# Kernel optimization log

Hardware: AMD Instinct MI355X
Metric: run time of the kernel (lower is better)

Reference implementation:

```python
import jax, jax.numpy as jnp
import numpy as np

TEMPERATURE = 0.5
NEG_FILL = -9e15


def setup_inputs() -> dict:
    key = jax.random.key(0)
    k1, k2 = jax.random.split(key)
    B, D = 8192, 128
    z_i = jax.random.normal(k1, (B, D), dtype=jnp.float32)
    z_j = jax.random.normal(k2, (B, D), dtype=jnp.float32)
    return {"z_i": z_i, "z_j": z_j}


def reference(z_i, z_j):
    B = z_i.shape[0]
    N = 2 * B
    z = jnp.concatenate([z_i, z_j], axis=0)              # [2B, D]
    sim = jnp.matmul(z, z.T) / TEMPERATURE               # [2B, 2B]
    # mask out self-similarity on the diagonal
    diag = jnp.eye(N, dtype=bool)
    sim = jnp.where(diag, NEG_FILL, sim)
    # positive pair of row k is row (k+B) mod 2B
    labels = jnp.concatenate([jnp.arange(B, N), jnp.arange(0, B)])
    # CrossEntropyLoss(reduction='sum'): sum_k logsumexp(sim[k]) - sim[k, labels[k]]
    lse = jax.nn.logsumexp(sim, axis=1)                  # [2B]
    pos = sim[jnp.arange(N), labels]                     # [2B]
    loss = jnp.sum(lse - pos)
    return loss / N
```

## Files before the change

### kernel.cpp

```cpp
#include <hip/hip_runtime.h>

#define TEMP    0.5f
#define LOG2E   1.4426950408889634f
#define C2      (LOG2E / TEMP)
#define MSHIFT  160.0f
#define LN2     0.6931471805599453f
#define NROWS   16384
#define BHALF   8192
#define DDIM    128
#define PREPB   2048

typedef __bf16 bf16x8 __attribute__((ext_vector_type(8)));
typedef float  f32x16 __attribute__((ext_vector_type(16)));
typedef float  f32x2  __attribute__((ext_vector_type(2)));

__device__ __forceinline__ float fexp2(float x) {
#if __has_builtin(__builtin_amdgcn_exp2f)
  return __builtin_amdgcn_exp2f(x);
#else
  return exp2f(x);
#endif
}

__device__ __forceinline__ unsigned short f2bf(float f) {
  unsigned int u = __float_as_uint(f);
  unsigned int r = (u + 0x7FFFu + ((u >> 16) & 1u)) >> 16;
  return (unsigned short)r;
}


__global__ void k_prep(const float* __restrict__ zi, const float* __restrict__ zj,
                       unsigned short* __restrict__ zbF,
                       float* __restrict__ S, float* __restrict__ Pp) {
  const int t   = blockIdx.x * 256 + threadIdx.x;
  const int row = t >> 5;
  const int k0  = (t & 31) * 4;
  const float* src = (row < BHALF) ? (zi + (size_t)row * DDIM)
                                   : (zj + (size_t)(row - BHALF) * DDIM);
  float4 v = *reinterpret_cast<const float4*>(src + k0);

  const int g = row >> 5, lo = row & 31, khi = k0 >> 3, j0 = k0 & 7;
  ushort4 o;
  o.x = f2bf(v.x); o.y = f2bf(v.y); o.z = f2bf(v.z); o.w = f2bf(v.w);
  *reinterpret_cast<ushort4*>(zbF + (size_t)g * 4096 + khi * 256 + lo * 8 + j0) = o;

  float dot = 0.f;
  if (row < BHALF) {
    float4 w = *reinterpret_cast<const float4*>(zj + (size_t)row * DDIM + k0);
    dot = fmaf(v.x, w.x, fmaf(v.y, w.y, fmaf(v.z, w.z, v.w * w.w)));
  }
#pragma unroll
  for (int m = 32; m >= 1; m >>= 1) dot += __shfl_xor(dot, m, 64);
  __shared__ float red[4];
  if ((threadIdx.x & 63) == 0) red[threadIdx.x >> 6] = dot;
  __syncthreads();
  if (threadIdx.x == 0) Pp[blockIdx.x] = red[0] + red[1] + red[2] + red[3];

  if (t < NROWS) S[t] = 0.f;
}

template <bool MASK>
__device__ __forceinline__ void expAcc(const f32x16& acc, f32x2& s, int d, int hi) {
#pragma unroll
  for (int k = 0; k < 8; ++k) {
    f32x2 u;
    u.x = acc[2 * k];
    u.y = acc[2 * k + 1];
    const f32x2 c2v = {C2, C2};
    const f32x2 msv = {-MSHIFT, -MSHIFT};
    u = __builtin_elementwise_fma(u, c2v, msv);
    f32x2 e;
    e.x = fexp2(u.x);
    e.y = fexp2(u.y);
    if (MASK) {
      const int r0 = 2 * k, r1 = 2 * k + 1;
      if (((r0 & 3) + 8 * (r0 >> 2) + 4 * hi) == d) e.x = 0.f;
      if (((r1 & 3) + 8 * (r1 >> 2) + 4 * hi) == d) e.y = 0.f;
    }
    s += e;
  }
}

__global__ __launch_bounds__(256, 2)
void k_main(const unsigned short* __restrict__ zbF, float* __restrict__ S) {
  const int wave = threadIdx.x >> 6;
  const int lane = threadIdx.x & 63;
  const int lo = lane & 31;
  const int hi = lane >> 5;
  const int rb = blockIdx.x & 31;
  const int cc = blockIdx.x >> 5;
  const int row0w = rb * 512 + wave * 128;

  bf16x8 b[4][8];
#pragma unroll
  for (int rt = 0; rt < 4; ++rt) {
    const unsigned short* bp = zbF + (size_t)((row0w >> 5) + rt) * 4096 + hi * 256 + lo * 8;
#pragma unroll
    for (int ks = 0; ks < 8; ++ks)
      b[rt][ks] = *reinterpret_cast<const bf16x8*>(bp + ks * 512);
  }

  const f32x16 kZ = {};
  f32x2 s[4];
#pragma unroll
  for (int rt = 0; rt < 4; ++rt) { s[rt].x = 0.f; s[rt].y = 0.f; }

  const int c0base = cc * 1024;
  const unsigned short* abase = zbF + (size_t)(c0base >> 5) * 4096 + hi * 256 + lo * 8;

  bf16x8 a[8];
#pragma unroll
  for (int ks = 0; ks < 8; ++ks)
    a[ks] = *reinterpret_cast<const bf16x8*>(abase + ks * 512);

  if (((blockIdx.x ^ wave) & 1) != 0) __builtin_amdgcn_s_sleep(4);

  for (int it = 0; it < 32; ++it) {
    const int c0 = c0base + it * 32;
    const int dr = c0 - row0w;
    const bool dg = (unsigned)dr < 128u;
    const int rtd = dg ? (dr >> 5) : -1;

    __builtin_amdgcn_s_setprio(1);
    f32x16 acc0 = __builtin_amdgcn_mfma_f32_32x32x16_bf16(a[0], b[0][0], kZ, 0, 0, 0);
    f32x16 acc1 = __builtin_amdgcn_mfma_f32_32x32x16_bf16(a[0], b[1][0], kZ, 0, 0, 0);
#pragma unroll
    for (int ks = 1; ks < 8; ++ks) {
      acc0 = __builtin_amdgcn_mfma_f32_32x32x16_bf16(a[ks], b[0][ks], acc0, 0, 0, 0);
      acc1 = __builtin_amdgcn_mfma_f32_32x32x16_bf16(a[ks], b[1][ks], acc1, 0, 0, 0);
    }
    __builtin_amdgcn_s_setprio(0);
    if (!dg) {
      expAcc<false>(acc0, s[0], -1, hi);
      expAcc<false>(acc1, s[1], -1, hi);
    } else {
      expAcc<true>(acc0, s[0], rtd == 0 ? lo : -1, hi);
      expAcc<true>(acc1, s[1], rtd == 1 ? lo : -1, hi);
    }

    __builtin_amdgcn_s_setprio(1);
    acc0 = __builtin_amdgcn_mfma_f32_32x32x16_bf16(a[0], b[2][0], kZ, 0, 0, 0);
    acc1 = __builtin_amdgcn_mfma_f32_32x32x16_bf16(a[0], b[3][0], kZ, 0, 0, 0);
#pragma unroll
    for (int ks = 1; ks < 8; ++ks) {
      acc0 = __builtin_amdgcn_mfma_f32_32x32x16_bf16(a[ks], b[2][ks], acc0, 0, 0, 0);
      acc1 = __builtin_amdgcn_mfma_f32_32x32x16_bf16(a[ks], b[3][ks], acc1, 0, 0, 0);
    }
    __builtin_amdgcn_s_setprio(0);

    if (it + 1 < 32) {
      const unsigned short* ap = abase + (size_t)(it + 1) * 4096;
#pragma unroll
      for (int ks = 0; ks < 8; ++ks)
        a[ks] = *reinterpret_cast<const bf16x8*>(ap + ks * 512);
    }

    if (!dg) {
      expAcc<false>(acc0, s[2], -1, hi);
      expAcc<false>(acc1, s[3], -1, hi);
    } else {
      expAcc<true>(acc0, s[2], rtd == 2 ? lo : -1, hi);
      expAcc<true>(acc1, s[3], rtd == 3 ? lo : -1, hi);
    }
  }

#pragma unroll
  for (int rt = 0; rt < 4; ++rt) {
    float v = s[rt].x + s[rt].y;
    v += __shfl_xor(v, 32, 64);
    if (hi == 0) atomicAdd(&S[row0w + rt * 32 + lo], v);
  }
}

__global__ void k_fin(const float* __restrict__ S, const float* __restrict__ Pp,
                      float* __restrict__ out) {
  const int t = threadIdx.x;
  float q = 0.f;
  for (int r = t; r < NROWS; r += 1024)
    q += LN2 * (MSHIFT + __log2f(S[r]));
  for (int r = t; r < PREPB; r += 1024)
    q -= 4.0f * Pp[r];
  __shared__ float red[1024];
  red[t] = q;
  __syncthreads();
  for (int s2 = 512; s2 > 0; s2 >>= 1) {
    if (t < s2) red[t] += red[t + s2];
    __syncthreads();
  }
  if (t == 0) out[0] = red[0] / (float)NROWS;
}

extern "C" void kernel_launch(void* const* d_in, const int* in_sizes, int n_in,
                              void* d_out, int out_size, void* d_ws, size_t ws_size,
                              hipStream_t stream) {
  const float* zi = (const float*)d_in[0];
  const float* zj = (const float*)d_in[1];
  unsigned short* zbF = (unsigned short*)d_ws;
  float* S  = (float*)((char*)d_ws + (size_t)NROWS * DDIM * 2);
  float* Pp = S + NROWS;
  float* out = (float*)d_out;

  hipLaunchKernelGGL(k_prep, dim3(PREPB), dim3(256), 0, stream, zi, zj, zbF, S, Pp);
  hipLaunchKernelGGL(k_main, dim3(512),  dim3(256), 0, stream, zbF, S);
  hipLaunchKernelGGL(k_fin,  dim3(1),    dim3(1024), 0, stream, S, Pp, out);
}
```

Baseline: 130.6 us.

## Fold scale into bf16 inputs, bias into MFMA init, and interleave MFMA with exp

The prep kernel now pre-scales z by sqrt(log2e/T) before bf16 conversion, and the MFMA accumulators start at -MSHIFT, so the per-element FMA before exp2 goes away. The main loop is restructured so three accumulators are live in a staggered order, with sched_group_barrier hints that interleave MFMA and VALU exp work. The last iteration is peeled to drop the reload branch, and s_sleep and setprio are removed. Scaling before bf16 rounding slightly changes numerics, and the scheduling hints may not give the intended overlap.

```diff
diff --git a/kernel.cpp b/kernel.cpp
--- a/kernel.cpp
+++ b/kernel.cpp
@@ -3,6 +3,7 @@
 #define TEMP    0.5f
 #define LOG2E   1.4426950408889634f
 #define C2      (LOG2E / TEMP)
+#define SQC2    1.6986436f
 #define MSHIFT  160.0f
 #define LN2     0.6931471805599453f
 #define NROWS   16384
@@ -41,7 +42,8 @@
 
   const int g = row >> 5, lo = row & 31, khi = k0 >> 3, j0 = k0 & 7;
   ushort4 o;
-  o.x = f2bf(v.x); o.y = f2bf(v.y); o.z = f2bf(v.z); o.w = f2bf(v.w);
+  o.x = f2bf(v.x * SQC2); o.y = f2bf(v.y * SQC2);
+  o.z = f2bf(v.z * SQC2); o.w = f2bf(v.w * SQC2);
   *reinterpret_cast<ushort4*>(zbF + (size_t)g * 4096 + khi * 256 + lo * 8 + j0) = o;
 
   float dot = 0.f;
@@ -59,25 +61,58 @@
   if (t < NROWS) S[t] = 0.f;
 }
 
+
 template <bool MASK>
 __device__ __forceinline__ void expAcc(const f32x16& acc, f32x2& s, int d, int hi) {
 #pragma unroll
   for (int k = 0; k < 8; ++k) {
-    f32x2 u;
-    u.x = acc[2 * k];
-    u.y = acc[2 * k + 1];
-    const f32x2 c2v = {C2, C2};
-    const f32x2 msv = {-MSHIFT, -MSHIFT};
-    u = __builtin_elementwise_fma(u, c2v, msv);
     f32x2 e;
-    e.x = fexp2(u.x);
-    e.y = fexp2(u.y);
+    e.x = fexp2(acc[2 * k]);
+    e.y = fexp2(acc[2 * k + 1]);
     if (MASK) {
       const int r0 = 2 * k, r1 = 2 * k + 1;
       if (((r0 & 3) + 8 * (r0 >> 2) + 4 * hi) == d) e.x = 0.f;
       if (((r1 & 3) + 8 * (r1 >> 2) + 4 * hi) == d) e.y = 0.f;
     }
     s += e;
+  }
+}
+
+#define MFMA_ __builtin_amdgcn_mfma_f32_32x32x16_bf16
+
+template <bool MASK, bool RELOAD>
+__device__ __forceinline__ void iterBody(bf16x8 (&a)[8], const bf16x8 (&b)[4][8],
+                                         const f32x16& kC, f32x2 (&s)[4],
+                                         const unsigned short* __restrict__ ap,
+                                         int d0, int d1, int d2, int d3, int hi) {
+  f32x16 acc0 = MFMA_(a[0], b[0][0], kC, 0, 0, 0);
+  f32x16 acc1 = MFMA_(a[0], b[1][0], kC, 0, 0, 0);
+#pragma unroll
+  for (int ks = 1; ks < 8; ++ks) {
+    acc0 = MFMA_(a[ks], b[0][ks], acc0, 0, 0, 0);
+    acc1 = MFMA_(a[ks], b[1][ks], acc1, 0, 0, 0);
+  }
+  f32x16 acc2 = MFMA_(a[0], b[2][0], kC, 0, 0, 0);
+#pragma unroll
+  for (int ks = 1; ks < 8; ++ks) acc2 = MFMA_(a[ks], b[2][ks], acc2, 0, 0, 0);
+  expAcc<MASK>(acc0, s[0], d0, hi);
+  acc0 = MFMA_(a[0], b[3][0], kC, 0, 0, 0);
+#pragma unroll
+  for (int ks = 1; ks < 8; ++ks) acc0 = MFMA_(a[ks], b[3][ks], acc0, 0, 0, 0);
+  expAcc<MASK>(acc1, s[1], d1, hi);
+  if constexpr (RELOAD) {
+#pragma unroll
+    for (int ks = 0; ks < 8; ++ks)
+      a[ks] = *reinterpret_cast<const bf16x8*>(ap + (size_t)ks * 512);
+  }
+  expAcc<MASK>(acc2, s[2], d2, hi);
+  expAcc<MASK>(acc0, s[3], d3, hi);
+
+  __builtin_amdgcn_sched_group_barrier(0x8, 16, 0);
+#pragma unroll
+  for (int i = 0; i < 16; ++i) {
+    __builtin_amdgcn_sched_group_barrier(0x8, 1, 0);
+    __builtin_amdgcn_sched_group_barrier(0x2, 3, 0);
   }
 }
 
@@ -100,7 +135,10 @@
       b[rt][ks] = *reinterpret_cast<const bf16x8*>(bp + ks * 512);
   }
 
-  const f32x16 kZ = {};
+  f32x16 kC;
+#pragma unroll
+  for (int r = 0; r < 16; ++r) kC[r] = -MSHIFT;
+
   f32x2 s[4];
 #pragma unroll
   for (int rt = 0; rt < 4; ++rt) { s[rt].x = 0.f; s[rt].y = 0.f; }
@@ -113,55 +151,29 @@
   for (int ks = 0; ks < 8; ++ks)
     a[ks] = *reinterpret_cast<const bf16x8*>(abase + ks * 512);
 
-  if (((blockIdx.x ^ wave) & 1) != 0) __builtin_amdgcn_s_sleep(4);
-
-  for (int it = 0; it < 32; ++it) {
+  for (int it = 0; it < 31; ++it) {
     const int c0 = c0base + it * 32;
     const int dr = c0 - row0w;
     const bool dg = (unsigned)dr < 128u;
-    const int rtd = dg ? (dr >> 5) : -1;
-
-    __builtin_amdgcn_s_setprio(1);
-    f32x16 acc0 = __builtin_amdgcn_mfma_f32_32x32x16_bf16(a[0], b[0][0], kZ, 0, 0, 0);
-    f32x16 acc1 = __builtin_amdgcn_mfma_f32_32x32x16_bf16(a[0], b[1][0], kZ, 0, 0, 0);
-#pragma unroll
-    for (int ks = 1; ks < 8; ++ks) {
-      acc0 = __builtin_amdgcn_mfma_f32_32x32x16_bf16(a[ks], b[0][ks], acc0, 0, 0, 0);
-      acc1 = __builtin_amdgcn_mfma_f32_32x32x16_bf16(a[ks], b[1][ks], acc1, 0, 0, 0);
-    }
-    __builtin_amdgcn_s_setprio(0);
-    if (!dg) {
-      expAcc<false>(acc0, s[0], -1, hi);
-      expAcc<false>(acc1, s[1], -1, hi);
-    } else {
-      expAcc<true>(acc0, s[0], rtd == 0 ? lo : -1, hi);
-      expAcc<true>(acc1, s[1], rtd == 1 ? lo : -1, hi);
-    }
-
-    __builtin_amdgcn_s_setprio(1);
-    acc0 = __builtin_amdgcn_mfma_f32_32x32x16_bf16(a[0], b[2][0], kZ, 0, 0, 0);
-    acc1 = __builtin_amdgcn_mfma_f32_32x32x16_bf16(a[0], b[3][0], kZ, 0, 0, 0);
-#pragma unroll
-    for (int ks = 1; ks < 8; ++ks) {
-      acc0 = __builtin_amdgcn_mfma_f32_32x32x16_bf16(a[ks], b[2][ks], acc0, 0, 0, 0);
-      acc1 = __builtin_amdgcn_mfma_f32_32x32x16_bf16(a[ks], b[3][ks], acc1, 0, 0, 0);
-    }
-    __builtin_amdgcn_s_setprio(0);
-
-    if (it + 1 < 32) {
-      const unsigned short* ap = abase + (size_t)(it + 1) * 4096;
-#pragma unroll
-      for (int ks = 0; ks < 8; ++ks)
-        a[ks] = *reinterpret_cast<const bf16x8*>(ap + ks * 512);
-    }
-
-    if (!dg) {
-      expAcc<false>(acc0, s[2], -1, hi);
-      expAcc<false>(acc1, s[3], -1, hi);
-    } else {
-      expAcc<true>(acc0, s[2], rtd == 2 ? lo : -1, hi);
-      expAcc<true>(acc1, s[3], rtd == 3 ? lo : -1, hi);
-    }
+    const int rtd = dr >> 5;
+    const unsigned short* apn = abase + (size_t)(it + 1) * 4096;
+    if (!dg)
+      iterBody<false, true>(a, b, kC, s, apn, -1, -1, -1, -1, hi);
+    else
+      iterBody<true, true>(a, b, kC, s, apn,
+                           rtd == 0 ? lo : -1, rtd == 1 ? lo : -1,
+                           rtd == 2 ? lo : -1, rtd == 3 ? lo : -1, hi);
+  }
+  {
+    const int dr = c0base + 31 * 32 - row0w;
+    const bool dg = (unsigned)dr < 128u;
+    const int rtd = dr >> 5;
+    if (!dg)
+      iterBody<false, false>(a, b, kC, s, abase, -1, -1, -1, -1, hi);
+    else
+      iterBody<true, false>(a, b, kC, s, abase,
+                            rtd == 0 ? lo : -1, rtd == 1 ? lo : -1,
+                            rtd == 2 ? lo : -1, rtd == 3 ? lo : -1, hi);
   }
 
 #pragma unroll
```

After: 164.3 us. +25.9%, slower.

## Fold temperature scale into bf16 inputs, shift into MFMA accumulator, fuse final reduction

Applied to the files above, without the earlier changes.

Inputs are pre-scaled by sqrt(log2e/T) before the bf16 conversion, and the MFMA accumulator starts at -MSHIFT. The dot products therefore come out ready for exp2, which removes the per-element FMA. The separate finalize kernel is replaced by a last-block-done pattern using an atomic counter inside the main kernel, saving one launch. The s_setprio and s_sleep staggering are removed. Scaling before rounding changes bf16 rounding slightly, and the final reduction now runs on 256 threads in one block.

```diff
diff --git a/kernel.cpp b/kernel.cpp
--- a/kernel.cpp
+++ b/kernel.cpp
@@ -3,12 +3,14 @@
 #define TEMP    0.5f
 #define LOG2E   1.4426950408889634f
 #define C2      (LOG2E / TEMP)
+#define SQC2    1.6986436f
 #define MSHIFT  160.0f
 #define LN2     0.6931471805599453f
 #define NROWS   16384
 #define BHALF   8192
 #define DDIM    128
 #define PREPB   2048
+#define MAINB   512
 
 typedef __bf16 bf16x8 __attribute__((ext_vector_type(8)));
 typedef float  f32x16 __attribute__((ext_vector_type(16)));
@@ -31,7 +33,8 @@
 
 __global__ void k_prep(const float* __restrict__ zi, const float* __restrict__ zj,
                        unsigned short* __restrict__ zbF,
-                       float* __restrict__ S, float* __restrict__ Pp) {
+                       float* __restrict__ S, float* __restrict__ Pp,
+                       unsigned int* __restrict__ cnt) {
   const int t   = blockIdx.x * 256 + threadIdx.x;
   const int row = t >> 5;
   const int k0  = (t & 31) * 4;
@@ -41,7 +44,8 @@
 
   const int g = row >> 5, lo = row & 31, khi = k0 >> 3, j0 = k0 & 7;
   ushort4 o;
-  o.x = f2bf(v.x); o.y = f2bf(v.y); o.z = f2bf(v.z); o.w = f2bf(v.w);
+  o.x = f2bf(v.x * SQC2); o.y = f2bf(v.y * SQC2);
+  o.z = f2bf(v.z * SQC2); o.w = f2bf(v.w * SQC2);
   *reinterpret_cast<ushort4*>(zbF + (size_t)g * 4096 + khi * 256 + lo * 8 + j0) = o;
 
   float dot = 0.f;
@@ -57,21 +61,16 @@
   if (threadIdx.x == 0) Pp[blockIdx.x] = red[0] + red[1] + red[2] + red[3];
 
   if (t < NROWS) S[t] = 0.f;
+  if (t == 0) cnt[0] = 0u;
 }
 
 template <bool MASK>
 __device__ __forceinline__ void expAcc(const f32x16& acc, f32x2& s, int d, int hi) {
 #pragma unroll
   for (int k = 0; k < 8; ++k) {
-    f32x2 u;
-    u.x = acc[2 * k];
-    u.y = acc[2 * k + 1];
-    const f32x2 c2v = {C2, C2};
-    const f32x2 msv = {-MSHIFT, -MSHIFT};
-    u = __builtin_elementwise_fma(u, c2v, msv);
     f32x2 e;
-    e.x = fexp2(u.x);
-    e.y = fexp2(u.y);
+    e.x = fexp2(acc[2 * k]);
+    e.y = fexp2(acc[2 * k + 1]);
     if (MASK) {
       const int r0 = 2 * k, r1 = 2 * k + 1;
       if (((r0 & 3) + 8 * (r0 >> 2) + 4 * hi) == d) e.x = 0.f;
@@ -81,8 +80,12 @@
   }
 }
 
+#define MFMA_ __builtin_amdgcn_mfma_f32_32x32x16_bf16
+
 __global__ __launch_bounds__(256, 2)
-void k_main(const unsigned short* __restrict__ zbF, float* __restrict__ S) {
+void k_main(const unsigned short* __restrict__ zbF, float* __restrict__ S,
+            const float* __restrict__ Pp, unsigned int* __restrict__ cnt,
+            float* __restrict__ out) {
   const int wave = threadIdx.x >> 6;
   const int lane = threadIdx.x & 63;
   const int lo = lane & 31;
@@ -100,7 +103,10 @@
       b[rt][ks] = *reinterpret_cast<const bf16x8*>(bp + ks * 512);
   }
 
-  const f32x16 kZ = {};
+  f32x16 kC;
+#pragma unroll
+  for (int r = 0; r < 16; ++r) kC[r] = -MSHIFT;
+
   f32x2 s[4];
 #pragma unroll
   for (int rt = 0; rt < 4; ++rt) { s[rt].x = 0.f; s[rt].y = 0.f; }
@@ -112,8 +118,6 @@
 #pragma unroll
   for (int ks = 0; ks < 8; ++ks)
     a[ks] = *reinterpret_cast<const bf16x8*>(abase + ks * 512);
-
-  if (((blockIdx.x ^ wave) & 1) != 0) __builtin_amdgcn_s_sleep(4);
 
   for (int it = 0; it < 32; ++it) {
     const int c0 = c0base + it * 32;
@@ -121,15 +125,13 @@
     const bool dg = (unsigned)dr < 128u;
     const int rtd = dg ? (dr >> 5) : -1;
 
-    __builtin_amdgcn_s_setprio(1);
-    f32x16 acc0 = __builtin_amdgcn_mfma_f32_32x32x16_bf16(a[0], b[0][0], kZ, 0, 0, 0);
-    f32x16 acc1 = __builtin_amdgcn_mfma_f32_32x32x16_bf16(a[0], b[1][0], kZ, 0, 0, 0);
+    f32x16 acc0 = MFMA_(a[0], b[0][0], kC, 0, 0, 0);
+    f32x16 acc1 = MFMA_(a[0], b[1][0], kC, 0, 0, 0);
 #pragma unroll
     for (int ks = 1; ks < 8; ++ks) {
-      acc0 = __builtin_amdgcn_mfma_f32_32x32x16_bf16(a[ks], b[0][ks], acc0, 0, 0, 0);
-      acc1 = __builtin_amdgcn_mfma_f32_32x32x16_bf16(a[ks], b[1][ks], acc1, 0, 0, 0);
-    }
-    __builtin_amdgcn_s_setprio(0);
+      acc0 = MFMA_(a[ks], b[0][ks], acc0, 0, 0, 0);
+      acc1 = MFMA_(a[ks], b[1][ks], acc1, 0, 0, 0);
+    }
     if (!dg) {
       expAcc<false>(acc0, s[0], -1, hi);
       expAcc<false>(acc1, s[1], -1, hi);
@@ -138,15 +140,13 @@
       expAcc<true>(acc1, s[1], rtd == 1 ? lo : -1, hi);
     }
 
-    __builtin_amdgcn_s_setprio(1);
-    acc0 = __builtin_amdgcn_mfma_f32_32x32x16_bf16(a[0], b[2][0], kZ, 0, 0, 0);
-    acc1 = __builtin_amdgcn_mfma_f32_32x32x16_bf16(a[0], b[3][0], kZ, 0, 0, 0);
+    acc0 = MFMA_(a[0], b[2][0], kC, 0, 0, 0);
+    acc1 = MFMA_(a[0], b[3][0], kC, 0, 0, 0);
 #pragma unroll
     for (int ks = 1; ks < 8; ++ks) {
-      acc0 = __builtin_amdgcn_mfma_f32_32x32x16_bf16(a[ks], b[2][ks], acc0, 0, 0, 0);
-      acc1 = __builtin_amdgcn_mfma_f32_32x32x16_bf16(a[ks], b[3][ks], acc1, 0, 0, 0);
-    }
-    __builtin_amdgcn_s_setprio(0);
+      acc0 = MFMA_(a[ks], b[2][ks], acc0, 0, 0, 0);
+      acc1 = MFMA_(a[ks], b[3][ks], acc1, 0, 0, 0);
+    }
 
     if (it + 1 < 32) {
       const unsigned short* ap = abase + (size_t)(it + 1) * 4096;
@@ -170,24 +170,36 @@
     v += __shfl_xor(v, 32, 64);
     if (hi == 0) atomicAdd(&S[row0w + rt * 32 + lo], v);
   }
-}
-
-__global__ void k_fin(const float* __restrict__ S, const float* __restrict__ Pp,
-                      float* __restrict__ out) {
-  const int t = threadIdx.x;
-  float q = 0.f;
-  for (int r = t; r < NROWS; r += 1024)
-    q += LN2 * (MSHIFT + __log2f(S[r]));
-  for (int r = t; r < PREPB; r += 1024)
-    q -= 4.0f * Pp[r];
-  __shared__ float red[1024];
-  red[t] = q;
+
+  __threadfence();
   __syncthreads();
-  for (int s2 = 512; s2 > 0; s2 >>= 1) {
-    if (t < s2) red[t] += red[t + s2];
+  __shared__ unsigned int lastFlag;
+  if (threadIdx.x == 0) {
+    unsigned int old = __hip_atomic_fetch_add(cnt, 1u, __ATOMIC_ACQ_REL,
+                                              __HIP_MEMORY_SCOPE_AGENT);
+    lastFlag = (old == (unsigned)(MAINB - 1)) ? 1u : 0u;
+  }
+  __syncthreads();
+  if (lastFlag) {
+    __threadfence();
+    const int t = threadIdx.x;
+    float q = 0.f;
+    for (int r = t; r < NROWS; r += 256) {
+      float sv = __hip_atomic_load(&S[r], __ATOMIC_RELAXED,
+                                   __HIP_MEMORY_SCOPE_AGENT);
+      q += LN2 * (MSHIFT + __log2f(sv));
+    }
+    for (int r = t; r < PREPB; r += 256)
+      q -= 4.0f * Pp[r];
+    __shared__ float red[256];
+    red[t] = q;
     __syncthreads();
-  }
-  if (t == 0) out[0] = red[0] / (float)NROWS;
+    for (int s2 = 128; s2 > 0; s2 >>= 1) {
+      if (t < s2) red[t] += red[t + s2];
+      __syncthreads();
+    }
+    if (t == 0) out[0] = red[0] / (float)NROWS;
+  }
 }
 
 extern "C" void kernel_launch(void* const* d_in, const int* in_sizes, int n_in,
@@ -198,9 +210,9 @@
   unsigned short* zbF = (unsigned short*)d_ws;
   float* S  = (float*)((char*)d_ws + (size_t)NROWS * DDIM * 2);
   float* Pp = S + NROWS;
+  unsigned int* cnt = (unsigned int*)(Pp + PREPB);
   float* out = (float*)d_out;
 
-  hipLaunchKernelGGL(k_prep, dim3(PREPB), dim3(256), 0, stream, zi, zj, zbF, S, Pp);
-  hipLaunchKernelGGL(k_main, dim3(512),  dim3(256), 0, stream, zbF, S);
-  hipLaunchKernelGGL(k_fin,  dim3(1),    dim3(1024), 0, stream, S, Pp, out);
-}
+  hipLaunchKernelGGL(k_prep, dim3(PREPB), dim3(256), 0, stream, zi, zj, zbF, S, Pp, cnt);
+  hipLaunchKernelGGL(k_main, dim3(MAINB), dim3(256), 0, stream, zbF, S, Pp, cnt, out);
+}
```

Measured after the change: 174.5 us. 1.34x slower.
